# Kernel optimization log

Measured on AMD Instinct MI355X. Metric: run time of the kernel, lower is better.

The kernel has to match this reference:

```python
import jax, jax.numpy as jnp
import numpy as np

WS = 7       # window_size
SHIFT = 3    # shift
NH = 4       # n_heads


def _rel_index(ws: int) -> np.ndarray:
    # matches torch.cartesian_prod(arange(ws), arange(ws)) ordering (second index fastest)
    coords = np.stack(np.meshgrid(np.arange(ws), np.arange(ws), indexing='ij'), -1).reshape(-1, 2)
    d = coords[:, None, :] - coords[None, :, :]
    idx = (d[..., 0] + ws - 1) * (2 * ws - 1) + d[..., 1] + ws - 1
    return idx.reshape(-1).astype(np.int32)  # [ws*ws*ws*ws]


def _ln(x, g, b, eps=1e-5):
    m = x.mean(-1, keepdims=True)
    v = ((x - m) ** 2).mean(-1, keepdims=True)
    return (x - m) / jnp.sqrt(v + eps) * g + b


def setup_inputs() -> dict:
    key = jax.random.key(0)
    ks = jax.random.split(key, 14)
    B, H, W, C = 64, 56, 56, 128
    hidden = int(C * 4.0)
    s = 0.02
    return {
        'x': jax.random.normal(ks[0], (B, H, W, C), jnp.float32),
        'norm1_g': jnp.ones((C,), jnp.float32),
        'norm1_b': jnp.zeros((C,), jnp.float32),
        'qkv_w': jax.random.normal(ks[1], (3 * C, C), jnp.float32) * s,
        'qkv_b': jnp.zeros((3 * C,), jnp.float32),
        'out_w': jax.random.normal(ks[2], (C, C), jnp.float32) * s,
        'out_b': jnp.zeros((C,), jnp.float32),
        'pe_table': jax.random.normal(ks[3], (NH, (2 * WS - 1) ** 2), jnp.float32) * s,
        'norm2_g': jnp.ones((C,), jnp.float32),
        'norm2_b': jnp.zeros((C,), jnp.float32),
        'mlp_w1': jax.random.normal(ks[4], (hidden, C), jnp.float32) * s,
        'mlp_b1': jnp.zeros((hidden,), jnp.float32),
        'mlp_w2': jax.random.normal(ks[5], (C, hidden), jnp.float32) * s,
        'mlp_b2': jnp.zeros((C,), jnp.float32),
    }


def reference(x, norm1_g, norm1_b, qkv_w, qkv_b, out_w, out_b, pe_table,
              norm2_g, norm2_b, mlp_w1, mlp_b1, mlp_w2, mlp_b2):
    B, H, W, C = x.shape
    nH, nW = H // WS, W // WS
    L = WS * WS
    hd = C // NH

    h = _ln(x, norm1_g, norm1_b)
    h = jnp.roll(h, (SHIFT, SHIFT), (1, 2))  # shifted windows (no inverse roll in source)

    # window partition: [B,H,W,C] -> [B*nH*nW, L, C]
    h = h.reshape(B, nH, WS, nW, WS, C).transpose(0, 1, 3, 2, 4, 5).reshape(B * nH * nW, L, C)

    qkv = h @ qkv_w.T + qkv_b  # [N, L, 3C]
    q, k, v = jnp.split(qkv, 3, axis=-1)
    to_heads = lambda t: t.reshape(-1, L, NH, hd).transpose(0, 2, 1, 3)  # [N,h,L,hd]
    q, k, v = to_heads(q), to_heads(k), to_heads(v)

    idx = jnp.asarray(_rel_index(WS))
    bias = pe_table[:, idx].reshape(NH, L, L)  # gathered relative position bias

    scores = jnp.einsum('nhqd,nhkd->nhqk', q, k) / jnp.sqrt(jnp.float32(hd)) + bias[None]
    attn = jax.nn.softmax(scores, axis=-1)
    o = jnp.einsum('nhqk,nhkd->nhqd', attn, v).transpose(0, 2, 1, 3).reshape(-1, L, C)
    o = o @ out_w.T + out_b

    # window unpartition: [B*nH*nW, L, C] -> [B,H,W,C]
    o = o.reshape(B, nH, nW, WS, WS, C).transpose(0, 1, 3, 2, 4, 5).reshape(B, H, W, C)

    h2 = _ln(o, norm2_g, norm2_b)
    y = jax.nn.gelu(h2 @ mlp_w1.T + mlp_b1, approximate=False) @ mlp_w2.T + mlp_b2
    return y
```

## Files before the change

### kernel.cpp

```cpp
#include <hip/hip_runtime.h>
#include <hip/hip_bf16.h>


#define NWIN 4096
#define STR 40
#define HB 7440
#define KOFF 2568
#define VOFF 5136

typedef __attribute__((ext_vector_type(8))) short s8v;
typedef __attribute__((ext_vector_type(4))) float f4v;

__device__ __forceinline__ void split2(float v, unsigned short& h, unsigned short& l) {
    unsigned int b = __float_as_uint(v);
    h = (unsigned short)(b >> 16);
    float hf = __uint_as_float(b & 0xFFFF0000u);
    __hip_bfloat16 lo = __float2bfloat16(v - hf);
    l = *reinterpret_cast<unsigned short*>(&lo);
}
__device__ __forceinline__ unsigned short bfr(float v) {
    __hip_bfloat16 h = __float2bfloat16(v);
    return *reinterpret_cast<unsigned short*>(&h);
}
__device__ __forceinline__ float b2f(unsigned short u) {
    return __uint_as_float((unsigned int)u << 16);
}

__global__ __launch_bounds__(256) void presplit_kernel(
    const float* __restrict__ qkvw, const float* __restrict__ outw,
    const float* __restrict__ w1, const float* __restrict__ w2,
    unsigned short* __restrict__ P)
{
    int i = blockIdx.x * 256 + threadIdx.x;
    float v; unsigned short* ph; unsigned short* pl;
    if (i < 49152) {
        v = qkvw[i];
        if (i < 16384) v *= 0.17677669529663687f;
        ph = P + i; pl = P + 49152 + i;
    } else if (i < 65536) {
        int j = i - 49152; v = outw[j];
        ph = P + 98304 + j; pl = P + 114688 + j;
    } else if (i < 131072) {
        int j = i - 65536; v = w1[j];
        ph = P + 131072 + j; pl = P + 196608 + j;
    } else if (i < 196608) {
        int j = i - 131072; v = w2[j];
        ph = P + 262144 + j; pl = P + 327680 + j;
    } else return;
    unsigned short h, l; split2(v, h, l);
    *ph = h; *pl = l;
}

__global__ __launch_bounds__(256) void ln_kernel(
    const float* __restrict__ inF, const unsigned short* __restrict__ inH,
    const float* __restrict__ g, const float* __restrict__ bta,
    unsigned short* __restrict__ outH, unsigned short* __restrict__ outL,
    int mode, int tbase)
{
    int tid = threadIdx.x;
    int wave = tid >> 6, lane = tid & 63;
    int local = blockIdx.x * 4 + wave;
    float v0, v1;
    if (mode == 0) {
        int t = tbase + local;
        int n = t / 49, l = t - n * 49;
        int b = n >> 6, wh = (n >> 3) & 7, ww = n & 7;
        int i = l / 7, j = l - i * 7;
        int hh = wh * 7 + i, wimg = ww * 7 + j;
        int sh = (hh + 53) % 56, sw = (wimg + 53) % 56;
        const float* ip = inF + (size_t)((b * 56 + sh) * 56 + sw) * 128;
        v0 = ip[lane]; v1 = ip[lane + 64];
    } else {
        size_t o = (size_t)local * 128;
        v0 = b2f(inH[o + lane]);
        v1 = b2f(inH[o + lane + 64]);
    }
    float s = v0 + v1, sq = v0 * v0 + v1 * v1;
    #pragma unroll
    for (int off = 32; off > 0; off >>= 1) { s += __shfl_xor(s, off); sq += __shfl_xor(sq, off); }
    float mean = s * (1.0f / 128.0f);
    float var  = sq * (1.0f / 128.0f) - mean * mean;
    float rstd = rsqrtf(var + 1e-5f);
    float r0 = (v0 - mean) * rstd * g[lane]      + bta[lane];
    float r1 = (v1 - mean) * rstd * g[lane + 64] + bta[lane + 64];
    size_t o = (size_t)local * 128;
    if (mode == 0) {
        unsigned short h0, l0, h1, l1;
        split2(r0, h0, l0); split2(r1, h1, l1);
        outH[o + lane] = h0; outH[o + lane + 64] = h1;
        outL[o + lane] = l0; outL[o + lane + 64] = l1;
    } else {
        outH[o + lane] = bfr(r0); outH[o + lane + 64] = bfr(r1);
    }
}

template<int ASPLIT>
__global__ __launch_bounds__(256) void gemm_t(
    const unsigned short* __restrict__ Agh, const unsigned short* __restrict__ Agl,
    const unsigned short* __restrict__ Wgh, const unsigned short* __restrict__ Wgl,
    const float* __restrict__ bias,
    float* __restrict__ OutF, unsigned short* __restrict__ OutH,
    unsigned short* __restrict__ OutV,
    int M, int N, int K, int mode, int tbase)
{
    __shared__ __align__(16) unsigned short Ah[64 * STR];
    __shared__ __align__(16) unsigned short Al[(ASPLIT ? 64 : 1) * STR];
    __shared__ __align__(16) unsigned short Wh[64 * STR];
    __shared__ __align__(16) unsigned short Wl[64 * STR];
    int tid = threadIdx.x;
    int wv = tid >> 6, ln = tid & 63;
    int wm = wv & 1, wn = wv >> 1;
    int fm = ln & 15, fq = ln >> 4;
    int m0 = blockIdx.y * 64, n0 = blockIdx.x * 64;
    int sr = tid >> 2, sk = (tid & 3) * 8;
    int arow = m0 + sr; if (arow >= M) arow = M - 1;
    const unsigned short* pAh = Agh + (size_t)arow * K + sk;
    const unsigned short* pAl = ASPLIT ? (Agl + (size_t)arow * K + sk) : nullptr;
    const unsigned short* pWh = Wgh + (size_t)(n0 + sr) * K + sk;
    const unsigned short* pWl = Wgl + (size_t)(n0 + sr) * K + sk;
    int so = sr * STR + sk;

    f4v acc[2][2] = {};
    s8v ra, rl, rwh, rwl;
    #define LOADK(k0) do { \
        ra  = *reinterpret_cast<const s8v*>(pAh + (k0)); \
        if (ASPLIT) rl = *reinterpret_cast<const s8v*>(pAl + (k0)); \
        rwh = *reinterpret_cast<const s8v*>(pWh + (k0)); \
        rwl = *reinterpret_cast<const s8v*>(pWl + (k0)); } while (0)
    LOADK(0);
    for (int k0 = 0; k0 < K; k0 += 32) {
        *reinterpret_cast<s8v*>(&Ah[so]) = ra;
        if (ASPLIT) *reinterpret_cast<s8v*>(&Al[so]) = rl;
        *reinterpret_cast<s8v*>(&Wh[so]) = rwh;
        *reinterpret_cast<s8v*>(&Wl[so]) = rwl;
        __syncthreads();
        if (k0 + 32 < K) LOADK(k0 + 32);
        s8v fah[2], fal[2], fbh[2], fbl[2];
        #pragma unroll
        for (int t = 0; t < 2; ++t) {
            int ao = (wm * 32 + t * 16 + fm) * STR + fq * 8;
            fah[t] = *reinterpret_cast<const s8v*>(&Ah[ao]);
            if (ASPLIT) fal[t] = *reinterpret_cast<const s8v*>(&Al[ao]);
            int bo = (wn * 32 + t * 16 + fm) * STR + fq * 8;
            fbh[t] = *reinterpret_cast<const s8v*>(&Wh[bo]);
            fbl[t] = *reinterpret_cast<const s8v*>(&Wl[bo]);
        }
        #pragma unroll
        for (int tm = 0; tm < 2; ++tm)
            #pragma unroll
            for (int tn = 0; tn < 2; ++tn) {
                acc[tm][tn] = __builtin_amdgcn_mfma_f32_16x16x32_bf16(fah[tm], fbh[tn], acc[tm][tn], 0, 0, 0);
                acc[tm][tn] = __builtin_amdgcn_mfma_f32_16x16x32_bf16(fah[tm], fbl[tn], acc[tm][tn], 0, 0, 0);
                if (ASPLIT)
                    acc[tm][tn] = __builtin_amdgcn_mfma_f32_16x16x32_bf16(fal[tm], fbh[tn], acc[tm][tn], 0, 0, 0);
            }
        __syncthreads();
    }
    #undef LOADK

    #pragma unroll
    for (int tm = 0; tm < 2; ++tm)
        #pragma unroll
        for (int tn = 0; tn < 2; ++tn) {
            int col = n0 + wn * 32 + tn * 16 + fm;
            float bv = bias[col];
            if (mode == 4 && col < 128) bv *= 0.17677669529663687f;
            #pragma unroll
            for (int r = 0; r < 4; ++r) {
                int m = m0 + wm * 32 + tm * 16 + fq * 4 + r;
                if (m >= M) continue;
                float v = acc[tm][tn][r] + bv;
                if (mode == 1) v = 0.5f * v * (1.0f + erff(v * 0.70710678118654752f));
                if (mode == 3) {
                    int t = tbase + m;
                    int n = t / 49, l = t - n * 49;
                    int b = n >> 6, wh_ = (n >> 3) & 7, ww = n & 7;
                    int i = l / 7, j = l - i * 7;
                    size_t orow = (size_t)((b * 56 + wh_ * 7 + i) * 56 + ww * 7 + j);
                    OutF[orow * N + col] = v;
                } else if (mode == 4) {
                    if (col < 256) {
                        OutH[(size_t)m * 256 + col] = bfr(v);
                    } else {
                        int dd = col - 256, hh = dd >> 5, d = dd & 31;
                        int win = m / 49, l2 = m - win * 49;
                        int kp = (l2 & 15) * 4 + (l2 >> 4);
                        OutV[((size_t)win * 128 + hh * 32 + d) * 64 + kp] = bfr(v);
                    }
                } else {
                    OutH[(size_t)m * N + col] = bfr(v);
                }
            }
        }
}

__global__ void bias_tab_kernel(const float* __restrict__ pe, float* __restrict__ tab) {
    int t = threadIdx.x;
    int h = t >> 6, ln = t & 63;
    int g = ln >> 4, c = ln & 15;
    for (int mt = 0; mt < 4; ++mt)
        for (int nt = 0; nt < 4; ++nt)
            for (int r = 0; r < 4; ++r) {
                int l1 = mt * 16 + g * 4 + r, l2 = nt * 16 + c;
                float b = 0.f;
                if (l1 < 49 && l2 < 49) {
                    int i1 = l1 / 7, j1 = l1 % 7, i2 = l2 / 7, j2 = l2 % 7;
                    b = pe[h * 169 + (i1 - i2 + 6) * 13 + (j1 - j2 + 6)];
                }
                tab[((h * 64 + ln) * 16 + mt * 4 + nt) * 4 + r] = b;
            }
}

__global__ __launch_bounds__(256) void attn_mfma(
    const unsigned short* __restrict__ qk,
    const unsigned short* __restrict__ vt,
    const float* __restrict__ btab,
    unsigned short* __restrict__ oH)
{
    __shared__ __align__(16) unsigned short lds[4 * HB];
    int tid = threadIdx.x;
    int win = blockIdx.x;
    const unsigned short* srcqk = qk + (size_t)win * 49 * 256;
    const unsigned short* srcv  = vt + (size_t)win * 8192;

    for (int idx = tid; idx < 1568; idx += 256) {
        int l2 = idx >> 5, c8 = idx & 31;
        int d8 = c8 * 8;
        s8v v8 = *reinterpret_cast<const s8v*>(srcqk + (size_t)l2 * 256 + d8);
        int sec = d8 >> 7, dd = d8 & 127, hh = dd >> 5, kk = dd & 31;
        *reinterpret_cast<s8v*>(&lds[hh * HB + (sec ? KOFF : 0) + l2 * 40 + kk]) = v8;
    }
    for (int idx = tid; idx < 1024; idx += 256) {
        int row = idx >> 3, j = idx & 7;
        s8v v8 = *reinterpret_cast<const s8v*>(srcv + (size_t)row * 64 + j * 8);
        int hh = row >> 5, d = row & 31;
        *reinterpret_cast<s8v*>(&lds[hh * HB + VOFF + d * 72 + j * 8]) = v8;
    }
    __syncthreads();
    for (int i = tid; i < 1920; i += 256) {
        int hh = i / 480, rem = i % 480, d = rem / 15, j = rem % 15;
        lds[hh * HB + VOFF + d * 72 + (j + 1) * 4 + 3] = 0;
    }
    __syncthreads();

    int h = tid >> 6, ln = tid & 63;
    int fm = ln & 15, fq = ln >> 4;
    int base = h * HB;

    s8v Qf[4], Kf[4];
    #pragma unroll
    for (int t = 0; t < 4; ++t) {
        Qf[t] = *reinterpret_cast<const s8v*>(&lds[base + (t * 16 + fm) * 40 + fq * 8]);
        Kf[t] = *reinterpret_cast<const s8v*>(&lds[base + KOFF + (t * 16 + fm) * 40 + fq * 8]);
    }
    f4v S[4][4] = {};
    #pragma unroll
    for (int mt = 0; mt < 4; ++mt)
        #pragma unroll
        for (int nt = 0; nt < 4; ++nt)
            S[mt][nt] = __builtin_amdgcn_mfma_f32_16x16x32_bf16(Qf[mt], Kf[nt], S[mt][nt], 0, 0, 0);
    #pragma unroll
    for (int mt = 0; mt < 4; ++mt)
        #pragma unroll
        for (int nt = 0; nt < 4; ++nt)
            S[mt][nt] += *reinterpret_cast<const f4v*>(&btab[((h * 64 + ln) * 16 + mt * 4 + nt) * 4]);

    float rcp[16];
    #pragma unroll
    for (int mt = 0; mt < 4; ++mt) {
        #pragma unroll
        for (int r = 0; r < 4; ++r) {
            float v0 = S[mt][0][r], v1 = S[mt][1][r], v2 = S[mt][2][r], v3 = S[mt][3][r];
            if (fm != 0) v3 = -1e30f;
            float mx = fmaxf(fmaxf(v0, v1), fmaxf(v2, v3));
            #pragma unroll
            for (int off = 1; off < 16; off <<= 1) mx = fmaxf(mx, __shfl_xor(mx, off));
            float e0 = __expf(v0 - mx), e1 = __expf(v1 - mx);
            float e2 = __expf(v2 - mx), e3 = __expf(v3 - mx);
            float sm = e0 + e1 + e2 + e3;
            #pragma unroll
            for (int off = 1; off < 16; off <<= 1) sm += __shfl_xor(sm, off);
            rcp[mt * 4 + r] = 1.0f / sm;
            int row = mt * 16 + fq * 4 + r;
            ushort4 pk = { bfr(e0), bfr(e1), bfr(e2), bfr(e3) };
            *reinterpret_cast<ushort4*>(&lds[base + row * 72 + fm * 4]) = pk;
        }
    }

    f4v O[4][2] = {};
    #pragma unroll
    for (int kt = 0; kt < 2; ++kt) {
        s8v Pf[4], Vf[2];
        #pragma unroll
        for (int mt = 0; mt < 4; ++mt)
            Pf[mt] = *reinterpret_cast<const s8v*>(&lds[base + (mt * 16 + fm) * 72 + kt * 32 + fq * 8]);
        #pragma unroll
        for (int nt = 0; nt < 2; ++nt)
            Vf[nt] = *reinterpret_cast<const s8v*>(&lds[base + VOFF + (nt * 16 + fm) * 72 + kt * 32 + fq * 8]);
        #pragma unroll
        for (int mt = 0; mt < 4; ++mt)
            #pragma unroll
            for (int nt = 0; nt < 2; ++nt)
                O[mt][nt] = __builtin_amdgcn_mfma_f32_16x16x32_bf16(Pf[mt], Vf[nt], O[mt][nt], 0, 0, 0);
    }

    size_t ob = (size_t)win * 49 * 128 + h * 32;
    #pragma unroll
    for (int mt = 0; mt < 4; ++mt)
        #pragma unroll
        for (int r = 0; r < 4; ++r) {
            int row = mt * 16 + fq * 4 + r;
            if (row < 49) {
                float sc = rcp[mt * 4 + r];
                #pragma unroll
                for (int nt = 0; nt < 2; ++nt)
                    oH[ob + (size_t)row * 128 + nt * 16 + fm] = bfr(O[mt][nt][r] * sc);
            }
        }
}

extern "C" void kernel_launch(void* const* d_in, const int* in_sizes, int n_in,
                              void* d_out, int out_size, void* d_ws, size_t ws_size,
                              hipStream_t stream) {
    const float* x    = (const float*)d_in[0];
    const float* n1g  = (const float*)d_in[1];
    const float* n1b  = (const float*)d_in[2];
    const float* qkvw = (const float*)d_in[3];
    const float* qkvb = (const float*)d_in[4];
    const float* outw = (const float*)d_in[5];
    const float* outb = (const float*)d_in[6];
    const float* pe   = (const float*)d_in[7];
    const float* n2g  = (const float*)d_in[8];
    const float* n2b  = (const float*)d_in[9];
    const float* w1   = (const float*)d_in[10];
    const float* b1   = (const float*)d_in[11];
    const float* w2   = (const float*)d_in[12];
    const float* b2   = (const float*)d_in[13];
    float* y = (float*)d_out;

    size_t wpc = NWIN;
    while (wpc > 8 && 851968 + wpc * 116736ULL > ws_size) wpc >>= 1;
    const int nchunks = (int)(NWIN / wpc);
    const size_t rows = wpc * 49;

    char* ws = (char*)d_ws;
    float* btab = (float*)ws;
    unsigned short* wpl = (unsigned short*)(ws + 65536);
    unsigned short* bufAh = (unsigned short*)(ws + 851968);
    unsigned short* bufAl = bufAh + rows * 128;
    unsigned short* bufQK = bufAl + rows * 128;
    unsigned short* bufV  = bufQK + rows * 256;
    unsigned short* bufH  = bufV + wpc * 8192;
    const int gy = (int)((rows + 63) / 64);

    presplit_kernel<<<768, 256, 0, stream>>>(qkvw, outw, w1, w2, wpl);
    bias_tab_kernel<<<1, 256, 0, stream>>>(pe, btab);

    for (int c = 0; c < nchunks; ++c) {
        int tbase = (int)(c * wpc * 49);
        ln_kernel<<<(int)(rows / 4), 256, 0, stream>>>(
            x, nullptr, n1g, n1b, bufAh, bufAl, 0, tbase);
        gemm_t<1><<<dim3(6, gy), 256, 0, stream>>>(
            bufAh, bufAl, wpl, wpl + 49152, qkvb,
            nullptr, bufQK, bufV, (int)rows, 384, 128, 4, 0);
        attn_mfma<<<(int)wpc, 256, 0, stream>>>(bufQK, bufV, btab, bufAh);
        gemm_t<0><<<dim3(2, gy), 256, 0, stream>>>(
            bufAh, nullptr, wpl + 98304, wpl + 114688, outb,
            nullptr, bufAl, nullptr, (int)rows, 128, 128, 0, 0);
        ln_kernel<<<(int)(rows / 4), 256, 0, stream>>>(
            nullptr, bufAl, n2g, n2b, bufAh, nullptr, 1, 0);
        gemm_t<0><<<dim3(8, gy), 256, 0, stream>>>(
            bufAh, nullptr, wpl + 131072, wpl + 196608, b1,
            nullptr, bufH, nullptr, (int)rows, 512, 128, 1, 0);
        gemm_t<0><<<dim3(2, gy), 256, 0, stream>>>(
            bufH, nullptr, wpl + 262144, wpl + 327680, b2,
            y, nullptr, nullptr, (int)rows, 128, 512, 3, tbase);
    }
}
```

Before: 786.9 us.

## Fuse out-proj with LayerNorm2 and MLP GEMMs into single kernels

```diff
diff --git a/kernel.cpp b/kernel.cpp
--- a/kernel.cpp
+++ b/kernel.cpp
@@ -3,7 +3,6 @@
 
 
 #define NWIN 4096
-#define STR 40
 #define HB 7440
 #define KOFF 2568
 #define VOFF 5136
@@ -21,9 +20,6 @@
 __device__ __forceinline__ unsigned short bfr(float v) {
     __hip_bfloat16 h = __float2bfloat16(v);
     return *reinterpret_cast<unsigned short*>(&h);
-}
-__device__ __forceinline__ float b2f(unsigned short u) {
-    return __uint_as_float((unsigned int)u << 16);
 }
 
 __global__ __launch_bounds__(256) void presplit_kernel(
@@ -52,29 +48,22 @@
 }
 
 __global__ __launch_bounds__(256) void ln_kernel(
-    const float* __restrict__ inF, const unsigned short* __restrict__ inH,
+    const float* __restrict__ inF,
     const float* __restrict__ g, const float* __restrict__ bta,
     unsigned short* __restrict__ outH, unsigned short* __restrict__ outL,
-    int mode, int tbase)
+    int tbase)
 {
     int tid = threadIdx.x;
     int wave = tid >> 6, lane = tid & 63;
     int local = blockIdx.x * 4 + wave;
-    float v0, v1;
-    if (mode == 0) {
-        int t = tbase + local;
-        int n = t / 49, l = t - n * 49;
-        int b = n >> 6, wh = (n >> 3) & 7, ww = n & 7;
-        int i = l / 7, j = l - i * 7;
-        int hh = wh * 7 + i, wimg = ww * 7 + j;
-        int sh = (hh + 53) % 56, sw = (wimg + 53) % 56;
-        const float* ip = inF + (size_t)((b * 56 + sh) * 56 + sw) * 128;
-        v0 = ip[lane]; v1 = ip[lane + 64];
-    } else {
-        size_t o = (size_t)local * 128;
-        v0 = b2f(inH[o + lane]);
-        v1 = b2f(inH[o + lane + 64]);
-    }
+    int t = tbase + local;
+    int n = t / 49, l = t - n * 49;
+    int b = n >> 6, wh = (n >> 3) & 7, ww = n & 7;
+    int i = l / 7, j = l - i * 7;
+    int hh = wh * 7 + i, wimg = ww * 7 + j;
+    int sh = (hh + 53) % 56, sw = (wimg + 53) % 56;
+    const float* ip = inF + (size_t)((b * 56 + sh) * 56 + sw) * 128;
+    float v0 = ip[lane], v1 = ip[lane + 64];
     float s = v0 + v1, sq = v0 * v0 + v1 * v1;
     #pragma unroll
     for (int off = 32; off > 0; off >>= 1) { s += __shfl_xor(s, off); sq += __shfl_xor(sq, off); }
@@ -83,67 +72,50 @@
     float rstd = rsqrtf(var + 1e-5f);
     float r0 = (v0 - mean) * rstd * g[lane]      + bta[lane];
     float r1 = (v1 - mean) * rstd * g[lane + 64] + bta[lane + 64];
+    unsigned short h0, l0, h1, l1;
+    split2(r0, h0, l0); split2(r1, h1, l1);
     size_t o = (size_t)local * 128;
-    if (mode == 0) {
-        unsigned short h0, l0, h1, l1;
-        split2(r0, h0, l0); split2(r1, h1, l1);
-        outH[o + lane] = h0; outH[o + lane + 64] = h1;
-        outL[o + lane] = l0; outL[o + lane + 64] = l1;
-    } else {
-        outH[o + lane] = bfr(r0); outH[o + lane + 64] = bfr(r1);
-    }
-}
-
-template<int ASPLIT>
-__global__ __launch_bounds__(256) void gemm_t(
+    outH[o + lane] = h0; outH[o + lane + 64] = h1;
+    outL[o + lane] = l0; outL[o + lane + 64] = l1;
+}
+
+__global__ __launch_bounds__(256) void qkv_gemm(
     const unsigned short* __restrict__ Agh, const unsigned short* __restrict__ Agl,
-    const unsigned short* __restrict__ Wgh, const unsigned short* __restrict__ Wgl,
+    const unsigned short* __restrict__ W,
     const float* __restrict__ bias,
-    float* __restrict__ OutF, unsigned short* __restrict__ OutH,
-    unsigned short* __restrict__ OutV,
-    int M, int N, int K, int mode, int tbase)
+    unsigned short* __restrict__ OutQK, unsigned short* __restrict__ OutV,
+    int M)
 {
-    __shared__ __align__(16) unsigned short Ah[64 * STR];
-    __shared__ __align__(16) unsigned short Al[(ASPLIT ? 64 : 1) * STR];
-    __shared__ __align__(16) unsigned short Wh[64 * STR];
-    __shared__ __align__(16) unsigned short Wl[64 * STR];
+    __shared__ __align__(16) unsigned short Ah[64 * 132];
+    __shared__ __align__(16) unsigned short Al[64 * 132];
     int tid = threadIdx.x;
+    int m0 = blockIdx.y * 64, n0 = blockIdx.x * 64;
+    for (int c = tid; c < 1024; c += 256) {
+        int row = c >> 4, c8 = (c & 15) * 8;
+        int ar = m0 + row; if (ar >= M) ar = M - 1;
+        *reinterpret_cast<s8v*>(&Ah[row * 132 + c8]) =
+            *reinterpret_cast<const s8v*>(Agh + (size_t)ar * 128 + c8);
+        *reinterpret_cast<s8v*>(&Al[row * 132 + c8]) =
+            *reinterpret_cast<const s8v*>(Agl + (size_t)ar * 128 + c8);
+    }
+    __syncthreads();
     int wv = tid >> 6, ln = tid & 63;
     int wm = wv & 1, wn = wv >> 1;
     int fm = ln & 15, fq = ln >> 4;
-    int m0 = blockIdx.y * 64, n0 = blockIdx.x * 64;
-    int sr = tid >> 2, sk = (tid & 3) * 8;
-    int arow = m0 + sr; if (arow >= M) arow = M - 1;
-    const unsigned short* pAh = Agh + (size_t)arow * K + sk;
-    const unsigned short* pAl = ASPLIT ? (Agl + (size_t)arow * K + sk) : nullptr;
-    const unsigned short* pWh = Wgh + (size_t)(n0 + sr) * K + sk;
-    const unsigned short* pWl = Wgl + (size_t)(n0 + sr) * K + sk;
-    int so = sr * STR + sk;
-
+    const unsigned short* Wh = W;
+    const unsigned short* Wl = W + 49152;
     f4v acc[2][2] = {};
-    s8v ra, rl, rwh, rwl;
-    #define LOADK(k0) do { \
-        ra  = *reinterpret_cast<const s8v*>(pAh + (k0)); \
-        if (ASPLIT) rl = *reinterpret_cast<const s8v*>(pAl + (k0)); \
-        rwh = *reinterpret_cast<const s8v*>(pWh + (k0)); \
-        rwl = *reinterpret_cast<const s8v*>(pWl + (k0)); } while (0)
-    LOADK(0);
-    for (int k0 = 0; k0 < K; k0 += 32) {
-        *reinterpret_cast<s8v*>(&Ah[so]) = ra;
-        if (ASPLIT) *reinterpret_cast<s8v*>(&Al[so]) = rl;
-        *reinterpret_cast<s8v*>(&Wh[so]) = rwh;
-        *reinterpret_cast<s8v*>(&Wl[so]) = rwl;
-        __syncthreads();
-        if (k0 + 32 < K) LOADK(k0 + 32);
+    #pragma unroll
+    for (int kk = 0; kk < 4; ++kk) {
         s8v fah[2], fal[2], fbh[2], fbl[2];
         #pragma unroll
         for (int t = 0; t < 2; ++t) {
-            int ao = (wm * 32 + t * 16 + fm) * STR + fq * 8;
+            int ao = (wm * 32 + t * 16 + fm) * 132 + kk * 32 + fq * 8;
             fah[t] = *reinterpret_cast<const s8v*>(&Ah[ao]);
-            if (ASPLIT) fal[t] = *reinterpret_cast<const s8v*>(&Al[ao]);
-            int bo = (wn * 32 + t * 16 + fm) * STR + fq * 8;
-            fbh[t] = *reinterpret_cast<const s8v*>(&Wh[bo]);
-            fbl[t] = *reinterpret_cast<const s8v*>(&Wl[bo]);
+            fal[t] = *reinterpret_cast<const s8v*>(&Al[ao]);
+            size_t wo = (size_t)(n0 + wn * 32 + t * 16 + fm) * 128 + kk * 32 + fq * 8;
+            fbh[t] = *reinterpret_cast<const s8v*>(Wh + wo);
+            fbl[t] = *reinterpret_cast<const s8v*>(Wl + wo);
         }
         #pragma unroll
         for (int tm = 0; tm < 2; ++tm)
@@ -151,44 +123,28 @@
             for (int tn = 0; tn < 2; ++tn) {
                 acc[tm][tn] = __builtin_amdgcn_mfma_f32_16x16x32_bf16(fah[tm], fbh[tn], acc[tm][tn], 0, 0, 0);
                 acc[tm][tn] = __builtin_amdgcn_mfma_f32_16x16x32_bf16(fah[tm], fbl[tn], acc[tm][tn], 0, 0, 0);
-                if (ASPLIT)
-                    acc[tm][tn] = __builtin_amdgcn_mfma_f32_16x16x32_bf16(fal[tm], fbh[tn], acc[tm][tn], 0, 0, 0);
-            }
-        __syncthreads();
-    }
-    #undef LOADK
-
+                acc[tm][tn] = __builtin_amdgcn_mfma_f32_16x16x32_bf16(fal[tm], fbh[tn], acc[tm][tn], 0, 0, 0);
+            }
+    }
     #pragma unroll
     for (int tm = 0; tm < 2; ++tm)
         #pragma unroll
         for (int tn = 0; tn < 2; ++tn) {
             int col = n0 + wn * 32 + tn * 16 + fm;
             float bv = bias[col];
-            if (mode == 4 && col < 128) bv *= 0.17677669529663687f;
+            if (col < 128) bv *= 0.17677669529663687f;
             #pragma unroll
             for (int r = 0; r < 4; ++r) {
                 int m = m0 + wm * 32 + tm * 16 + fq * 4 + r;
                 if (m >= M) continue;
                 float v = acc[tm][tn][r] + bv;
-                if (mode == 1) v = 0.5f * v * (1.0f + erff(v * 0.70710678118654752f));
-                if (mode == 3) {
-                    int t = tbase + m;
-                    int n = t / 49, l = t - n * 49;
-                    int b = n >> 6, wh_ = (n >> 3) & 7, ww = n & 7;
-                    int i = l / 7, j = l - i * 7;
-                    size_t orow = (size_t)((b * 56 + wh_ * 7 + i) * 56 + ww * 7 + j);
-                    OutF[orow * N + col] = v;
-                } else if (mode == 4) {
-                    if (col < 256) {
-                        OutH[(size_t)m * 256 + col] = bfr(v);
-                    } else {
-                        int dd = col - 256, hh = dd >> 5, d = dd & 31;
-                        int win = m / 49, l2 = m - win * 49;
-                        int kp = (l2 & 15) * 4 + (l2 >> 4);
-                        OutV[((size_t)win * 128 + hh * 32 + d) * 64 + kp] = bfr(v);
-                    }
+                if (col < 256) {
+                    OutQK[(size_t)m * 256 + col] = bfr(v);
                 } else {
-                    OutH[(size_t)m * N + col] = bfr(v);
+                    int dd = col - 256, hh = dd >> 5, d = dd & 31;
+                    int win = m / 49, l2 = m - win * 49;
+                    int kp = (l2 & 15) * 4 + (l2 >> 4);
+                    OutV[((size_t)win * 128 + hh * 32 + d) * 64 + kp] = bfr(v);
                 }
             }
         }
@@ -315,6 +271,201 @@
                 #pragma unroll
                 for (int nt = 0; nt < 2; ++nt)
                     oH[ob + (size_t)row * 128 + nt * 16 + fm] = bfr(O[mt][nt][r] * sc);
+            }
+        }
+}
+
+__global__ __launch_bounds__(256) void proj_ln(
+    const unsigned short* __restrict__ Ag,
+    const unsigned short* __restrict__ W,
+    const float* __restrict__ bias,
+    const float* __restrict__ g, const float* __restrict__ bta,
+    unsigned short* __restrict__ Out, int M)
+{
+    __shared__ __align__(16) unsigned short As[64 * 132];
+    __shared__ float red[2][2][64];
+    int tid = threadIdx.x;
+    int m0 = blockIdx.x * 64;
+    for (int c = tid; c < 1024; c += 256) {
+        int row = c >> 4, c8 = (c & 15) * 8;
+        int ar = m0 + row; if (ar >= M) ar = M - 1;
+        *reinterpret_cast<s8v*>(&As[row * 132 + c8]) =
+            *reinterpret_cast<const s8v*>(Ag + (size_t)ar * 128 + c8);
+    }
+    __syncthreads();
+    int wv = tid >> 6, ln = tid & 63;
+    int wm = wv & 1, wn = wv >> 1;
+    int fm = ln & 15, fq = ln >> 4;
+    const unsigned short* Wh = W;
+    const unsigned short* Wl = W + 16384;
+    f4v acc[2][4] = {};
+    #pragma unroll
+    for (int kk = 0; kk < 4; ++kk) {
+        s8v fa[2];
+        #pragma unroll
+        for (int t = 0; t < 2; ++t)
+            fa[t] = *reinterpret_cast<const s8v*>(&As[(wm * 32 + t * 16 + fm) * 132 + kk * 32 + fq * 8]);
+        #pragma unroll
+        for (int tn = 0; tn < 4; ++tn) {
+            size_t wo = (size_t)(wn * 64 + tn * 16 + fm) * 128 + kk * 32 + fq * 8;
+            s8v bh = *reinterpret_cast<const s8v*>(Wh + wo);
+            s8v bl = *reinterpret_cast<const s8v*>(Wl + wo);
+            #pragma unroll
+            for (int tm = 0; tm < 2; ++tm) {
+                acc[tm][tn] = __builtin_amdgcn_mfma_f32_16x16x32_bf16(fa[tm], bh, acc[tm][tn], 0, 0, 0);
+                acc[tm][tn] = __builtin_amdgcn_mfma_f32_16x16x32_bf16(fa[tm], bl, acc[tm][tn], 0, 0, 0);
+            }
+        }
+    }
+    float sumv[2][4], sqv[2][4];
+    #pragma unroll
+    for (int tm = 0; tm < 2; ++tm)
+        #pragma unroll
+        for (int r = 0; r < 4; ++r) {
+            float s = 0.f, q = 0.f;
+            #pragma unroll
+            for (int tn = 0; tn < 4; ++tn) {
+                float v = acc[tm][tn][r] + bias[wn * 64 + tn * 16 + fm];
+                acc[tm][tn][r] = v;
+                s += v; q += v * v;
+            }
+            #pragma unroll
+            for (int off = 1; off < 16; off <<= 1) { s += __shfl_xor(s, off); q += __shfl_xor(q, off); }
+            sumv[tm][r] = s; sqv[tm][r] = q;
+        }
+    if (fm == 0) {
+        #pragma unroll
+        for (int tm = 0; tm < 2; ++tm)
+            #pragma unroll
+            for (int r = 0; r < 4; ++r) {
+                int row = wm * 32 + tm * 16 + fq * 4 + r;
+                red[wn][0][row] = sumv[tm][r];
+                red[wn][1][row] = sqv[tm][r];
+            }
+    }
+    __syncthreads();
+    #pragma unroll
+    for (int tm = 0; tm < 2; ++tm)
+        #pragma unroll
+        for (int r = 0; r < 4; ++r) {
+            int row = wm * 32 + tm * 16 + fq * 4 + r;
+            int m = m0 + row;
+            float s = red[0][0][row] + red[1][0][row];
+            float q = red[0][1][row] + red[1][1][row];
+            float mean = s * (1.0f / 128.0f);
+            float var  = q * (1.0f / 128.0f) - mean * mean;
+            float rstd = rsqrtf(var + 1e-5f);
+            if (m < M) {
+                #pragma unroll
+                for (int tn = 0; tn < 4; ++tn) {
+                    int n = wn * 64 + tn * 16 + fm;
+                    float o = (acc[tm][tn][r] - mean) * rstd * g[n] + bta[n];
+                    Out[(size_t)m * 128 + n] = bfr(o);
+                }
+            }
+        }
+}
+
+__global__ __launch_bounds__(256) void mlp_fused(
+    const unsigned short* __restrict__ Ag,
+    const unsigned short* __restrict__ W1,
+    const unsigned short* __restrict__ W2,
+    const float* __restrict__ b1, const float* __restrict__ b2,
+    float* __restrict__ y, int M, int tbase)
+{
+    __shared__ __align__(16) unsigned short As[64 * 132];
+    __shared__ __align__(16) unsigned short Hs[2][64 * 68];
+    int tid = threadIdx.x;
+    int m0 = blockIdx.x * 64;
+    for (int c = tid; c < 1024; c += 256) {
+        int row = c >> 4, c8 = (c & 15) * 8;
+        int ar = m0 + row; if (ar >= M) ar = M - 1;
+        *reinterpret_cast<s8v*>(&As[row * 132 + c8]) =
+            *reinterpret_cast<const s8v*>(Ag + (size_t)ar * 128 + c8);
+    }
+    __syncthreads();
+    int wv = tid >> 6, ln = tid & 63;
+    int wm = wv & 1, wn = wv >> 1;
+    int fm = ln & 15, fq = ln >> 4;
+    const unsigned short* W1h = W1;
+    const unsigned short* W1l = W1 + 65536;
+    const unsigned short* W2h = W2;
+    const unsigned short* W2l = W2 + 65536;
+    f4v acc2[2][4] = {};
+    for (int j = 0; j < 8; ++j) {
+        int jb = j & 1;
+        f4v acc1[2][2] = {};
+        #pragma unroll
+        for (int kk = 0; kk < 4; ++kk) {
+            s8v fa[2], bh[2], bl[2];
+            #pragma unroll
+            for (int t = 0; t < 2; ++t) {
+                fa[t] = *reinterpret_cast<const s8v*>(&As[(wm * 32 + t * 16 + fm) * 132 + kk * 32 + fq * 8]);
+                size_t wo = (size_t)(j * 64 + wn * 32 + t * 16 + fm) * 128 + kk * 32 + fq * 8;
+                bh[t] = *reinterpret_cast<const s8v*>(W1h + wo);
+                bl[t] = *reinterpret_cast<const s8v*>(W1l + wo);
+            }
+            #pragma unroll
+            for (int tm = 0; tm < 2; ++tm)
+                #pragma unroll
+                for (int tn = 0; tn < 2; ++tn) {
+                    acc1[tm][tn] = __builtin_amdgcn_mfma_f32_16x16x32_bf16(fa[tm], bh[tn], acc1[tm][tn], 0, 0, 0);
+                    acc1[tm][tn] = __builtin_amdgcn_mfma_f32_16x16x32_bf16(fa[tm], bl[tn], acc1[tm][tn], 0, 0, 0);
+                }
+        }
+        #pragma unroll
+        for (int tm = 0; tm < 2; ++tm)
+            #pragma unroll
+            for (int tn = 0; tn < 2; ++tn) {
+                int nl = wn * 32 + tn * 16 + fm;
+                float bv = b1[j * 64 + nl];
+                #pragma unroll
+                for (int r = 0; r < 4; ++r) {
+                    float v = acc1[tm][tn][r] + bv;
+                    v = 0.5f * v * (1.0f + erff(v * 0.70710678118654752f));
+                    int m = wm * 32 + tm * 16 + fq * 4 + r;
+                    Hs[jb][m * 68 + nl] = bfr(v);
+                }
+            }
+        __syncthreads();
+        #pragma unroll
+        for (int kt = 0; kt < 2; ++kt) {
+            s8v hf[2], wh[4], wl[4];
+            #pragma unroll
+            for (int t = 0; t < 2; ++t)
+                hf[t] = *reinterpret_cast<const s8v*>(&Hs[jb][(wm * 32 + t * 16 + fm) * 68 + kt * 32 + fq * 8]);
+            #pragma unroll
+            for (int tn = 0; tn < 4; ++tn) {
+                size_t wo = (size_t)(wn * 64 + tn * 16 + fm) * 512 + j * 64 + kt * 32 + fq * 8;
+                wh[tn] = *reinterpret_cast<const s8v*>(W2h + wo);
+                wl[tn] = *reinterpret_cast<const s8v*>(W2l + wo);
+            }
+            #pragma unroll
+            for (int tm = 0; tm < 2; ++tm)
+                #pragma unroll
+                for (int tn = 0; tn < 4; ++tn) {
+                    acc2[tm][tn] = __builtin_amdgcn_mfma_f32_16x16x32_bf16(hf[tm], wh[tn], acc2[tm][tn], 0, 0, 0);
+                    acc2[tm][tn] = __builtin_amdgcn_mfma_f32_16x16x32_bf16(hf[tm], wl[tn], acc2[tm][tn], 0, 0, 0);
+                }
+        }
+    }
+    #pragma unroll
+    for (int tm = 0; tm < 2; ++tm)
+        #pragma unroll
+        for (int tn = 0; tn < 4; ++tn) {
+            int col = wn * 64 + tn * 16 + fm;
+            float bv = b2[col];
+            #pragma unroll
+            for (int r = 0; r < 4; ++r) {
+                int m = m0 + wm * 32 + tm * 16 + fq * 4 + r;
+                if (m >= M) continue;
+                float v = acc2[tm][tn][r] + bv;
+                int t = tbase + m;
+                int n = t / 49, l = t - n * 49;
+                int b = n >> 6, wh_ = (n >> 3) & 7, ww = n & 7;
+                int i = l / 7, jj = l - i * 7;
+                size_t orow = (size_t)((b * 56 + wh_ * 7 + i) * 56 + ww * 7 + jj);
+                y[orow * 128 + col] = v;
             }
         }
 }
@@ -339,7 +490,7 @@
     float* y = (float*)d_out;
 
     size_t wpc = NWIN;
-    while (wpc > 8 && 851968 + wpc * 116736ULL > ws_size) wpc >>= 1;
+    while (wpc > 8 && 851968 + wpc * 66560ULL > ws_size) wpc >>= 1;
     const int nchunks = (int)(NWIN / wpc);
     const size_t rows = wpc * 49;
 
@@ -350,7 +501,6 @@
     unsigned short* bufAl = bufAh + rows * 128;
     unsigned short* bufQK = bufAl + rows * 128;
     unsigned short* bufV  = bufQK + rows * 256;
-    unsigned short* bufH  = bufV + wpc * 8192;
     const int gy = (int)((rows + 63) / 64);
 
     presplit_kernel<<<768, 256, 0, stream>>>(qkvw, outw, w1, w2, wpl);
@@ -358,22 +508,10 @@
 
     for (int c = 0; c < nchunks; ++c) {
         int tbase = (int)(c * wpc * 49);
-        ln_kernel<<<(int)(rows / 4), 256, 0, stream>>>(
-            x, nullptr, n1g, n1b, bufAh, bufAl, 0, tbase);
-        gemm_t<1><<<dim3(6, gy), 256, 0, stream>>>(
-            bufAh, bufAl, wpl, wpl + 49152, qkvb,
-            nullptr, bufQK, bufV, (int)rows, 384, 128, 4, 0);
+        ln_kernel<<<(int)(rows / 4), 256, 0, stream>>>(x, n1g, n1b, bufAh, bufAl, tbase);
+        qkv_gemm<<<dim3(6, gy), 256, 0, stream>>>(bufAh, bufAl, wpl, qkvb, bufQK, bufV, (int)rows);
         attn_mfma<<<(int)wpc, 256, 0, stream>>>(bufQK, bufV, btab, bufAh);
-        gemm_t<0><<<dim3(2, gy), 256, 0, stream>>>(
-            bufAh, nullptr, wpl + 98304, wpl + 114688, outb,
-            nullptr, bufAl, nullptr, (int)rows, 128, 128, 0, 0);
-        ln_kernel<<<(int)(rows / 4), 256, 0, stream>>>(
-            nullptr, bufAl, n2g, n2b, bufAh, nullptr, 1, 0);
-        gemm_t<0><<<dim3(8, gy), 256, 0, stream>>>(
-            bufAh, nullptr, wpl + 131072, wpl + 196608, b1,
-            nullptr, bufH, nullptr, (int)rows, 512, 128, 1, 0);
-        gemm_t<0><<<dim3(2, gy), 256, 0, stream>>>(
-            bufH, nullptr, wpl + 262144, wpl + 327680, b2,
-            y, nullptr, nullptr, (int)rows, 128, 512, 3, tbase);
-    }
-}
+        proj_ln<<<gy, 256, 0, stream>>>(bufAh, wpl + 98304, outb, n2g, n2b, bufAl, (int)rows);
+        mlp_fused<<<gy, 256, 0, stream>>>(bufAl, wpl + 131072, wpl + 262144, b1, b2, y, (int)rows, tbase);
+    }
+}
```

New measurement: 1.038 ms. +32.0%, slower.
